# Kernel tuning notes

Measured on AMD Instinct MI355X. Metric: run time of the kernel, lower is better.

Reference implementation:

```python
import jax, jax.numpy as jnp
import numpy as np

N_NODE = 100000
DEPTH = 10
N_EDGE = 1600000
D_FEAT = 32
BASE_ALPHA = 1.0


def setup_inputs() -> dict:
    key = jax.random.key(0)
    k1, k2 = jax.random.split(key)
    x = jax.random.normal(k1, (N_NODE, D_FEAT), dtype=jnp.float32)
    edge_index = jax.random.randint(k2, (2, N_EDGE), 0, N_NODE, dtype=jnp.int64)
    edge_attr = jnp.ones((N_EDGE,), dtype=jnp.float32)
    # alphas init: min(1/alpha, 1) = 1.0 for each of depth+1 coefficients
    alphas = jnp.ones((DEPTH + 1,), dtype=jnp.float32)
    return {"x": x, "edge_index": edge_index, "edge_attr": edge_attr, "alphas": alphas}


def reference(x, edge_index, edge_attr, alphas):
    n_node = x.shape[0]
    row, col = edge_index[0], edge_index[1]

    # GCN normalization: val = deg^-1/2[row] * w * deg^-1/2[col]
    deg = jax.ops.segment_sum(jnp.ones_like(edge_attr), row, num_segments=n_node)
    deg = jnp.where(deg < 0.5, deg + 1.0, deg)
    dinv = deg ** -0.5
    val = dinv[row] * edge_attr * dinv[col]  # (E,)

    def adj_mul(h):  # sparse A @ h via gather + segment_sum (coalesce-equivalent)
        return jax.ops.segment_sum(val[:, None] * h[col], row, num_segments=n_node)

    alphas_t = BASE_ALPHA * jnp.tanh(alphas)  # (depth+1,)

    # PowerConv (monomial basis): x_0 = x; x_L = alpha_L * (A @ x_{L-1})
    xs = [x]
    for L in range(1, DEPTH + 1):
        xs.append(alphas_t[L] * adj_mul(xs[-1]))
    return jnp.stack(xs, axis=1)  # (n_node, depth+1, d_feat)
```

## Files before the change

kernel.cpp:

```cpp
#include <hip/hip_runtime.h>
#include <math.h>

#define N_NODE 100000
#define DEPTH  10
#define N_EDGE 1600000
#define D_FEAT 32
#define D_OUT  ((DEPTH + 1) * D_FEAT)
#define NB_SCAN ((N_NODE + 255) / 256)

typedef float        f32x4 __attribute__((ext_vector_type(4)));
typedef unsigned int u32x4 __attribute__((ext_vector_type(4)));
typedef int          i32x2 __attribute__((ext_vector_type(2)));

__device__ inline unsigned short f32_to_bf16(float f) {
    unsigned int b = __float_as_uint(f);
    unsigned int r = (b + 0x7FFFu + ((b >> 16) & 1u)) >> 16;
    return (unsigned short)r;
}
__device__ inline unsigned int pack_bf16x2(float lo, float hi) {
    return (unsigned int)f32_to_bf16(lo) | ((unsigned int)f32_to_bf16(hi) << 16);
}

__global__ void count_kernel(const int* __restrict__ row, int* __restrict__ cnt, int E) {
    int e = blockIdx.x * blockDim.x + threadIdx.x;
    if (e < E) atomicAdd(&cnt[row[e]], 1);
}

__device__ inline int wave_incl_scan(int v) {
    int lane = threadIdx.x & 63;
    #pragma unroll
    for (int off = 1; off < 64; off <<= 1) {
        int t = __shfl_up(v, off, 64);
        if (lane >= off) v += t;
    }
    return v;
}

__global__ void blockscan_kernel(const int* __restrict__ cnt, int* __restrict__ rowStart,
                                 int* __restrict__ blockSums, int n) {
    __shared__ int partials[4];
    int i = blockIdx.x * 256 + threadIdx.x;
    int v = (i < n) ? cnt[i] : 0;
    int incl = wave_incl_scan(v);
    int wid = threadIdx.x >> 6, lane = threadIdx.x & 63;
    if (lane == 63) partials[wid] = incl;
    __syncthreads();
    int woff = 0;
    #pragma unroll
    for (int w = 0; w < 4; ++w) woff += (w < wid) ? partials[w] : 0;
    if (i < n) rowStart[i] = woff + incl - v;
    if (threadIdx.x == 255) blockSums[blockIdx.x] = woff + incl;
}

__global__ void scansums_kernel(int* __restrict__ blockSums, int nb) {
    __shared__ int partials[8];
    int i = threadIdx.x;
    int v = (i < nb) ? blockSums[i] : 0;
    int incl = wave_incl_scan(v);
    int wid = i >> 6, lane = i & 63;
    if (lane == 63) partials[wid] = incl;
    __syncthreads();
    int woff = 0;
    #pragma unroll
    for (int w = 0; w < 8; ++w) woff += (w < wid) ? partials[w] : 0;
    if (i < nb) blockSums[i] = woff + incl - v;
    if (i == 511) blockSums[nb] = woff + incl;
}

__global__ void addoffs_kernel(int* __restrict__ rowStart, const int* __restrict__ blockSums,
                               int n, int nb) {
    int i = blockIdx.x * 256 + threadIdx.x;
    if (i < n)  rowStart[i] += blockSums[i >> 8];
    if (i == n) rowStart[n] = blockSums[nb];
}

__global__ void dinv_kernel(const int* __restrict__ cnt, float* __restrict__ dinv, int n) {
    int i = blockIdx.x * blockDim.x + threadIdx.x;
    if (i < n) {
        float d = (float)cnt[i];
        if (d < 0.5f) d += 1.0f;
        dinv[i] = 1.0f / sqrtf(d);
    }
}

__global__ void scatter_kernel(const int* __restrict__ row, const int* __restrict__ col,
                               const float* __restrict__ eattr,
                               const int* __restrict__ rowStart, int* __restrict__ cnt,
                               const float* __restrict__ dinv,
                               i32x2* __restrict__ csr, int E) {
    int e = blockIdx.x * blockDim.x + threadIdx.x;
    if (e < E) {
        int r = row[e], c = col[e];
        int p = rowStart[r] + atomicSub(&cnt[r], 1) - 1;
        float val = dinv[r] * eattr[e] * dinv[c];
        i32x2 ent; ent.x = c; ent.y = __float_as_int(val);
        __builtin_nontemporal_store(ent, &csr[p]);
    }
}

__global__ void alpha_kernel(const float* __restrict__ alphas, float* __restrict__ alphaT) {
    int i = threadIdx.x;
    if (i <= DEPTH) alphaT[i] = tanhf(alphas[i]);
}

__global__ void copyx_kernel(const f32x4* __restrict__ x4, f32x4* __restrict__ out4,
                             unsigned int* __restrict__ h0) {
    int i = blockIdx.x * blockDim.x + threadIdx.x;
    if (i < N_NODE * 8) {
        int node = i >> 3, q = i & 7;
        f32x4 v = x4[i];
        __builtin_nontemporal_store(v, &out4[(size_t)node * 88 + q]);
        h0[i * 2]     = pack_bf16x2(v.x, v.y);
        h0[i * 2 + 1] = pack_bf16x2(v.z, v.w);
    }
}

__global__ __launch_bounds__(256) void spmm_kernel(const int* __restrict__ rowStart,
                                                   const i32x2* __restrict__ csr,
                                                   const float* __restrict__ alphaT,
                                                   int L,
                                                   const u32x4* __restrict__ h_prev,
                                                   u32x4* __restrict__ h_cur,
                                                   f32x4* __restrict__ out4) {
    int rowid = (int)((blockIdx.x * 256 + threadIdx.x) >> 6);
    if (rowid >= N_NODE) return;
    int lane = threadIdx.x & 63;
    int s = lane >> 2;
    int q = lane & 3;

    int start = rowStart[rowid];
    int end   = rowStart[rowid + 1];

    float acc[8] = {0.f, 0.f, 0.f, 0.f, 0.f, 0.f, 0.f, 0.f};
    for (int e = start + s; e < end; e += 16) {
        i32x2 cv = __builtin_nontemporal_load(&csr[e]);
        float v  = __int_as_float(cv.y);
        u32x4 h  = h_prev[(size_t)cv.x * 4 + q];
        acc[0] += v * __uint_as_float(h.x << 16);
        acc[1] += v * __uint_as_float(h.x & 0xFFFF0000u);
        acc[2] += v * __uint_as_float(h.y << 16);
        acc[3] += v * __uint_as_float(h.y & 0xFFFF0000u);
        acc[4] += v * __uint_as_float(h.z << 16);
        acc[5] += v * __uint_as_float(h.z & 0xFFFF0000u);
        acc[6] += v * __uint_as_float(h.w << 16);
        acc[7] += v * __uint_as_float(h.w & 0xFFFF0000u);
    }

    #pragma unroll
    for (int m = 4; m < 64; m <<= 1) {
        #pragma unroll
        for (int k = 0; k < 8; ++k) acc[k] += __shfl_xor(acc[k], m, 64);
    }

    if (s == 0) {
        float a = alphaT[L];
        #pragma unroll
        for (int k = 0; k < 8; ++k) acc[k] *= a;
        size_t ob = (size_t)rowid * 88 + L * 8 + q * 2;
        f32x4 o0; o0.x = acc[0]; o0.y = acc[1]; o0.z = acc[2]; o0.w = acc[3];
        f32x4 o1; o1.x = acc[4]; o1.y = acc[5]; o1.z = acc[6]; o1.w = acc[7];
        __builtin_nontemporal_store(o0, &out4[ob]);
        __builtin_nontemporal_store(o1, &out4[ob + 1]);
        if (L < DEPTH) {
            u32x4 hh;
            hh.x = pack_bf16x2(acc[0], acc[1]);
            hh.y = pack_bf16x2(acc[2], acc[3]);
            hh.z = pack_bf16x2(acc[4], acc[5]);
            hh.w = pack_bf16x2(acc[6], acc[7]);
            __builtin_nontemporal_store(hh, &h_cur[(size_t)rowid * 4 + q]);
        }
    }
}

extern "C" void kernel_launch(void* const* d_in, const int* in_sizes, int n_in,
                              void* d_out, int out_size, void* d_ws, size_t ws_size,
                              hipStream_t stream) {
    const float* x      = (const float*)d_in[0];
    const int*   eidx   = (const int*)d_in[1];
    const float* eattr  = (const float*)d_in[2];
    const float* alphas = (const float*)d_in[3];
    float* out = (float*)d_out;

    const int* row = eidx;
    const int* col = eidx + N_EDGE;

    char* p = (char*)d_ws;
    auto alloc = [&](size_t bytes) { char* r = p; p += (bytes + 255) & ~(size_t)255; return (void*)r; };
    int*   cnt       = (int*)  alloc((size_t)N_NODE * 4);
    int*   rowStart  = (int*)  alloc((size_t)(N_NODE + 1) * 4);
    int*   blockSums = (int*)  alloc((size_t)(NB_SCAN + 1) * 4);
    float* dinv      = (float*)alloc((size_t)N_NODE * 4);
    float* alphaT    = (float*)alloc(64);
    u32x4* h0        = (u32x4*)alloc((size_t)N_NODE * 64);
    u32x4* h1        = (u32x4*)alloc((size_t)N_NODE * 64);
    i32x2* csr       = (i32x2*)alloc((size_t)N_EDGE * 8);
    (void)ws_size; (void)in_sizes; (void)n_in; (void)out_size;

    (void)hipMemsetAsync(cnt, 0, (size_t)N_NODE * 4, stream);

    const int TB = 256;
    int eBlocks = (N_EDGE + TB - 1) / TB;
    int nBlocks = (N_NODE + TB - 1) / TB;

    count_kernel<<<eBlocks, TB, 0, stream>>>(row, cnt, N_EDGE);
    blockscan_kernel<<<NB_SCAN, TB, 0, stream>>>(cnt, rowStart, blockSums, N_NODE);
    scansums_kernel<<<1, 512, 0, stream>>>(blockSums, NB_SCAN);
    addoffs_kernel<<<(N_NODE + 1 + TB - 1) / TB, TB, 0, stream>>>(rowStart, blockSums, N_NODE, NB_SCAN);
    dinv_kernel<<<nBlocks, TB, 0, stream>>>(cnt, dinv, N_NODE);
    scatter_kernel<<<eBlocks, TB, 0, stream>>>(row, col, eattr, rowStart, cnt, dinv, csr, N_EDGE);
    alpha_kernel<<<1, 64, 0, stream>>>(alphas, alphaT);
    copyx_kernel<<<(N_NODE * 8 + TB - 1) / TB, TB, 0, stream>>>((const f32x4*)x, (f32x4*)out,
                                                                (unsigned int*)h0);

    int spmmBlocks = (N_NODE * 64 + TB - 1) / TB;
    for (int L = 1; L <= DEPTH; ++L) {
        const u32x4* hp = (L & 1) ? h0 : h1;
        u32x4*       hc = (L & 1) ? h1 : h0;
        spmm_kernel<<<spmmBlocks, TB, 0, stream>>>(rowStart, csr, alphaT, L, hp, hc,
                                                   (f32x4*)out);
    }
}
```

Measured before the change: 593.6 us.

## Split feature dimension into two halves processed by separate SpMM chains

Splits the 32-wide bf16 feature vectors into two 16-feature halves stored in separate arrays and runs the full 10-layer SpMM chain twice, once per half. Each gathered row is half the size (32 bytes), so the working set of h_prev (3.2MB instead of 6.4MB) fits better in L2/MALL, raising the cache hit rate of the random gathers. In exchange the CSR structure and row pointers are read twice as often and there are twice as many kernel launches, with 32 edges per wave per iteration instead of 16.

```diff
diff --git a/kernel.cpp b/kernel.cpp
--- a/kernel.cpp
+++ b/kernel.cpp
@@ -104,38 +104,40 @@
 }
 
 __global__ void copyx_kernel(const f32x4* __restrict__ x4, f32x4* __restrict__ out4,
-                             unsigned int* __restrict__ h0) {
+                             unsigned int* __restrict__ h0A, unsigned int* __restrict__ h0B) {
     int i = blockIdx.x * blockDim.x + threadIdx.x;
     if (i < N_NODE * 8) {
         int node = i >> 3, q = i & 7;
         f32x4 v = x4[i];
         __builtin_nontemporal_store(v, &out4[(size_t)node * 88 + q]);
-        h0[i * 2]     = pack_bf16x2(v.x, v.y);
-        h0[i * 2 + 1] = pack_bf16x2(v.z, v.w);
-    }
-}
-
-__global__ __launch_bounds__(256) void spmm_kernel(const int* __restrict__ rowStart,
-                                                   const i32x2* __restrict__ csr,
-                                                   const float* __restrict__ alphaT,
-                                                   int L,
-                                                   const u32x4* __restrict__ h_prev,
-                                                   u32x4* __restrict__ h_cur,
-                                                   f32x4* __restrict__ out4) {
+        unsigned int* hh = (q < 4) ? h0A : h0B;
+        int w = (q & 3) * 2;
+        hh[(size_t)node * 8 + w]     = pack_bf16x2(v.x, v.y);
+        hh[(size_t)node * 8 + w + 1] = pack_bf16x2(v.z, v.w);
+    }
+}
+
+__global__ __launch_bounds__(256) void spmm_half(const int* __restrict__ rowStart,
+                                                 const i32x2* __restrict__ csr,
+                                                 const float* __restrict__ alphaT,
+                                                 int L, int half,
+                                                 const u32x4* __restrict__ h_prev,
+                                                 u32x4* __restrict__ h_cur,
+                                                 f32x4* __restrict__ out4) {
     int rowid = (int)((blockIdx.x * 256 + threadIdx.x) >> 6);
     if (rowid >= N_NODE) return;
     int lane = threadIdx.x & 63;
-    int s = lane >> 2;
-    int q = lane & 3;
+    int s = lane >> 1;
+    int q = lane & 1;
 
     int start = rowStart[rowid];
     int end   = rowStart[rowid + 1];
 
     float acc[8] = {0.f, 0.f, 0.f, 0.f, 0.f, 0.f, 0.f, 0.f};
-    for (int e = start + s; e < end; e += 16) {
+    for (int e = start + s; e < end; e += 32) {
         i32x2 cv = __builtin_nontemporal_load(&csr[e]);
         float v  = __int_as_float(cv.y);
-        u32x4 h  = h_prev[(size_t)cv.x * 4 + q];
+        u32x4 h  = h_prev[(size_t)cv.x * 2 + q];
         acc[0] += v * __uint_as_float(h.x << 16);
         acc[1] += v * __uint_as_float(h.x & 0xFFFF0000u);
         acc[2] += v * __uint_as_float(h.y << 16);
@@ -147,7 +149,7 @@
     }
 
     #pragma unroll
-    for (int m = 4; m < 64; m <<= 1) {
+    for (int m = 2; m < 64; m <<= 1) {
         #pragma unroll
         for (int k = 0; k < 8; ++k) acc[k] += __shfl_xor(acc[k], m, 64);
     }
@@ -156,7 +158,7 @@
         float a = alphaT[L];
         #pragma unroll
         for (int k = 0; k < 8; ++k) acc[k] *= a;
-        size_t ob = (size_t)rowid * 88 + L * 8 + q * 2;
+        size_t ob = (size_t)rowid * 88 + L * 8 + half * 4 + q * 2;
         f32x4 o0; o0.x = acc[0]; o0.y = acc[1]; o0.z = acc[2]; o0.w = acc[3];
         f32x4 o1; o1.x = acc[4]; o1.y = acc[5]; o1.z = acc[6]; o1.w = acc[7];
         __builtin_nontemporal_store(o0, &out4[ob]);
@@ -167,7 +169,7 @@
             hh.y = pack_bf16x2(acc[2], acc[3]);
             hh.z = pack_bf16x2(acc[4], acc[5]);
             hh.w = pack_bf16x2(acc[6], acc[7]);
-            __builtin_nontemporal_store(hh, &h_cur[(size_t)rowid * 4 + q]);
+            h_cur[(size_t)rowid * 2 + q] = hh;
         }
     }
 }
@@ -191,8 +193,10 @@
     int*   blockSums = (int*)  alloc((size_t)(NB_SCAN + 1) * 4);
     float* dinv      = (float*)alloc((size_t)N_NODE * 4);
     float* alphaT    = (float*)alloc(64);
-    u32x4* h0        = (u32x4*)alloc((size_t)N_NODE * 64);
-    u32x4* h1        = (u32x4*)alloc((size_t)N_NODE * 64);
+    u32x4* h0A       = (u32x4*)alloc((size_t)N_NODE * 32);
+    u32x4* h0B       = (u32x4*)alloc((size_t)N_NODE * 32);
+    u32x4* t0        = (u32x4*)alloc((size_t)N_NODE * 32);
+    u32x4* t1        = (u32x4*)alloc((size_t)N_NODE * 32);
     i32x2* csr       = (i32x2*)alloc((size_t)N_EDGE * 8);
     (void)ws_size; (void)in_sizes; (void)n_in; (void)out_size;
 
@@ -210,13 +214,17 @@
     scatter_kernel<<<eBlocks, TB, 0, stream>>>(row, col, eattr, rowStart, cnt, dinv, csr, N_EDGE);
     alpha_kernel<<<1, 64, 0, stream>>>(alphas, alphaT);
     copyx_kernel<<<(N_NODE * 8 + TB - 1) / TB, TB, 0, stream>>>((const f32x4*)x, (f32x4*)out,
-                                                                (unsigned int*)h0);
+                                                                (unsigned int*)h0A,
+                                                                (unsigned int*)h0B);
 
     int spmmBlocks = (N_NODE * 64 + TB - 1) / TB;
-    for (int L = 1; L <= DEPTH; ++L) {
-        const u32x4* hp = (L & 1) ? h0 : h1;
-        u32x4*       hc = (L & 1) ? h1 : h0;
-        spmm_kernel<<<spmmBlocks, TB, 0, stream>>>(rowStart, csr, alphaT, L, hp, hc,
-                                                   (f32x4*)out);
-    }
-}
+    for (int half = 0; half < 2; ++half) {
+        const u32x4* h0 = (half == 0) ? h0A : h0B;
+        for (int L = 1; L <= DEPTH; ++L) {
+            const u32x4* hp = (L == 1) ? h0 : ((L & 1) ? t1 : t0);
+            u32x4*       hc = (L & 1) ? t0 : t1;
+            spmm_half<<<spmmBlocks, TB, 0, stream>>>(rowStart, csr, alphaT, L, half,
+                                                     hp, hc, (f32x4*)out);
+        }
+    }
+}
```

After: 1.039 ms. 1.75x slower.
